# Optimization experiments

Measured on AMD Instinct MI355X. Metric: run time of the kernel, lower is better.

Reference implementation:

```python
import jax, jax.numpy as jnp
from jax import lax
import numpy as np
import math

B_SZ, SEQ, D_MODEL = 2, 2048, 2048
D_INNER, D_STATE, D_CONV, HEADS, P, CHUNK = 4096, 128, 4, 64, 64, 128
CONV_DIM = D_INNER + 2 * D_STATE
D_IN_PROJ = 2 * D_INNER + 2 * D_STATE + HEADS


def setup_inputs() -> dict:
    key = jax.random.key(0)
    ks = jax.random.split(key, 6)
    hidden_states = jax.random.normal(ks[0], (B_SZ, SEQ, D_MODEL), jnp.float32)
    W_in = jax.random.normal(ks[1], (D_IN_PROJ, D_MODEL), jnp.float32) * 0.02
    W_conv = jax.random.normal(ks[2], (CONV_DIM, 1, D_CONV), jnp.float32) * 0.2
    b_conv = jnp.zeros((CONV_DIM,), jnp.float32)
    A_log = jnp.log(jnp.arange(1, HEADS + 1, dtype=jnp.float32))
    D = jnp.ones((HEADS,), jnp.float32)
    # dt_bias init as in the torch module
    dt = jnp.exp(jax.random.uniform(ks[3], (HEADS,)) * (math.log(0.1) - math.log(0.001)) + math.log(0.001))
    dt = jnp.clip(dt, 1e-4, None)
    dt_bias = dt + jnp.log(-jnp.expm1(-dt))
    norm_weight = jnp.ones((D_INNER,), jnp.float32)
    W_out = jax.random.normal(ks[4], (D_MODEL, D_INNER), jnp.float32) * 0.02
    return {"hidden_states": hidden_states, "W_in": W_in, "W_conv": W_conv, "b_conv": b_conv,
            "A_log": A_log, "D": D, "dt_bias": dt_bias, "norm_weight": norm_weight, "W_out": W_out}


def _mamba2_core(hidden_states, W_in, W_conv, b_conv, A_log, D, dt_bias, norm_weight, W_out):
    Bsz, L, _ = hidden_states.shape
    NC = L // CHUNK
    zxbcdt = hidden_states @ W_in.T                         # [B,L,d_in_proj]
    z = zxbcdt[..., :D_INNER]
    xBC = zxbcdt[..., D_INNER:D_INNER + CONV_DIM]
    dt = zxbcdt[..., -HEADS:]
    # causal depthwise conv1d over sequence
    xc = jnp.swapaxes(xBC, 1, 2)                            # [B,C,L]
    xc = lax.conv_general_dilated(xc, W_conv, (1,), [(D_CONV - 1, 0)],
                                  feature_group_count=CONV_DIM,
                                  dimension_numbers=('NCH', 'OIH', 'NCH'))
    xc = xc + b_conv[None, :, None]
    xBC = jax.nn.silu(jnp.swapaxes(xc, 1, 2))               # [B,L,conv_dim]
    x = xBC[..., :D_INNER]
    Bm = xBC[..., D_INNER:D_INNER + D_STATE]                # num_groups=1
    Cm = xBC[..., -D_STATE:]
    dt = jax.nn.softplus(dt + dt_bias)                      # [B,L,H]; dt_limit (0,inf) is a no-op
    A = -jnp.exp(A_log)                                     # [H]
    # --- chunked SSD scan (chunk_size = CHUNK), same math as torch_ssm ---
    xch = x.reshape(Bsz, NC, CHUNK, HEADS, P)
    dtc = dt.reshape(Bsz, NC, CHUNK, HEADS)
    Bc = Bm.reshape(Bsz, NC, CHUNK, D_STATE)
    Cc = Cm.reshape(Bsz, NC, CHUNK, D_STATE)
    u = xch * dtc[..., None]                                # [b,c,l,h,p]
    dA = dtc * A                                            # [b,c,l,h]
    dA_cs = jnp.cumsum(dA, axis=2)                          # [b,c,l,h]
    # within-chunk causal attention-like term
    seg = dA_cs[:, :, :, None, :] - dA_cs[:, :, None, :, :] # [b,c,l,s,h]
    mask = jnp.tril(jnp.ones((CHUNK, CHUNK), bool))
    Lmat = jnp.exp(jnp.where(mask[None, None, :, :, None], seg, -jnp.inf))
    CB = jnp.einsum('bcln,bcsn->bcls', Cc, Bc)
    M = CB[..., None] * Lmat                                # [b,c,l,s,h]
    Y_diag = jnp.einsum('bclsh,bcshp->bclhp', M, u)
    # per-chunk final states
    decay_states = jnp.exp(dA_cs[:, :, -1:, :] - dA_cs)     # [b,c,l,h]
    states = jnp.einsum('bcln,bclh,bclhp->bchpn', Bc, decay_states, u)
    chunk_decay = jnp.exp(dA_cs[:, :, -1, :])               # [b,c,h]
    # inter-chunk recurrence over NC chunks
    def step(h, inp):
        st, cd = inp                                        # [b,h,p,n], [b,h]
        h_new = h * cd[:, :, None, None] + st
        return h_new, h                                     # emit state at chunk start
    sts = jnp.moveaxis(states, 1, 0)
    cds = jnp.moveaxis(chunk_decay, 1, 0)
    h0 = jnp.zeros((Bsz, HEADS, P, D_STATE), hidden_states.dtype)
    _, h_starts = lax.scan(step, h0, (sts, cds))
    h_starts = jnp.moveaxis(h_starts, 0, 1)                 # [b,c,h,p,n]
    state_decay_out = jnp.exp(dA_cs)                        # [b,c,l,h]
    Y_off = jnp.einsum('bcln,bclh,bchpn->bclhp', Cc, state_decay_out, h_starts)
    Y = Y_diag + Y_off + D[None, None, None, :, None] * xch
    y = Y.reshape(Bsz, L, D_INNER)
    # gated RMSNorm (gate first, then norm; group_size == d_inner)
    yg = y * jax.nn.silu(z)
    var = jnp.mean(yg * yg, axis=-1, keepdims=True)
    y = yg * lax.rsqrt(var + 1e-5) * norm_weight
    return y @ W_out.T


def reference(hidden_states, W_in, W_conv, b_conv, A_log, D, dt_bias, norm_weight, W_out):
    return _mamba2_core(hidden_states, W_in, W_conv, b_conv, A_log, D, dt_bias, norm_weight, W_out)
```

## Files before the change

kernel.cpp:

```cpp
#include <hip/hip_runtime.h>
#include <hip/hip_bf16.h>
#include <stdint.h>

typedef __bf16 bf16;
typedef __bf16 bf16x8 __attribute__((ext_vector_type(8)));
typedef __bf16 bf16x4 __attribute__((ext_vector_type(4)));
typedef float f32x4v __attribute__((ext_vector_type(4)));

#define SEQ    2048
#define DMODEL 2048
#define DI     4096
#define NH     64
#define PDIM   64
#define CHUNKL 128
#define NCH    16
#define CONVD  4352
#define DPROJ  8512
#define ZLD    8704
#define NTOK   4096
#define LP     136

__device__ __forceinline__ float sigmoid_f(float x){ return 1.f/(1.f+expf(-x)); }
__device__ __forceinline__ float silu_f(float x){ return x*sigmoid_f(x); }
__device__ __forceinline__ float softplus_f(float x){ return x > 20.f ? x : log1pf(expf(x)); }

__global__ __launch_bounds__(256) void cvt_all_kernel(const float* __restrict__ hs,
                                                      const float* __restrict__ W_in,
                                                      const float* __restrict__ W_out,
                                                      bf16* __restrict__ hsb,
                                                      bf16* __restrict__ winb,
                                                      bf16* __restrict__ woutb){
    int blk = blockIdx.x;
    if (blk < 8192){
        int i = (blk*256 + threadIdx.x)*4;
        float4 v = *(const float4*)&hs[i];
        bf16x4 o; o[0]=(bf16)v.x; o[1]=(bf16)v.y; o[2]=(bf16)v.z; o[3]=(bf16)v.w;
        *(bf16x4*)&hsb[i] = o;
    } else if (blk < 25600){
        int i = ((blk-8192)*256 + threadIdx.x)*4;
        int r = i >> 11;
        bf16x4 o;
        if (r < DPROJ){
            float4 v = *(const float4*)&W_in[i];
            o[0]=(bf16)v.x; o[1]=(bf16)v.y; o[2]=(bf16)v.z; o[3]=(bf16)v.w;
        } else {
            o[0]=(bf16)0.f; o[1]=(bf16)0.f; o[2]=(bf16)0.f; o[3]=(bf16)0.f;
        }
        *(bf16x4*)&winb[i] = o;
    } else {
        int i = ((blk-25600)*256 + threadIdx.x)*4;
        float4 v = *(const float4*)&W_out[i];
        bf16x4 o; o[0]=(bf16)v.x; o[1]=(bf16)v.y; o[2]=(bf16)v.z; o[3]=(bf16)v.w;
        *(bf16x4*)&woutb[i] = o;
    }
}

#define READ_A(BUFP, QM)                                                               \
    {                                                                                  \
        _Pragma("unroll")                                                              \
        for (int i=0;i<4;i++)                                                          \
            _Pragma("unroll")                                                          \
            for (int k2=0;k2<2;k2++)                                                   \
                af[i][k2] = *(const bf16x8*)&(BUFP)[aoff[i][k2] + (QM)*8192];          \
    }

#define READ_B(BUFP, QN, BFR)                                                          \
    {                                                                                  \
        _Pragma("unroll")                                                              \
        for (int nf=0;nf<2;nf++)                                                       \
            _Pragma("unroll")                                                          \
            for (int k2=0;k2<2;k2++)                                                   \
                BFR[nf][k2] = *(const bf16x8*)&(BUFP)[boff[nf][k2] + (QN)*8192];       \
    }

#define MMA_Q(QM, QN, BFR)                                                             \
    {                                                                                  \
        __builtin_amdgcn_s_setprio(1);                                                 \
        _Pragma("unroll")                                                              \
        for (int i=0;i<4;i++)                                                          \
            _Pragma("unroll")                                                          \
            for (int nf=0;nf<2;nf++)                                                   \
                _Pragma("unroll")                                                      \
                for (int k2=0;k2<2;k2++)                                               \
                    acc[(QM)*4+i][(QN)*2+nf] = __builtin_amdgcn_mfma_f32_16x16x32_bf16( \
                        af[i][k2], BFR[nf][k2], acc[(QM)*4+i][(QN)*2+nf], 0,0,0);      \
        __builtin_amdgcn_s_setprio(0);                                                 \
    }

#define SBAR() do { __builtin_amdgcn_sched_barrier(0);                                 \
                    __builtin_amdgcn_s_barrier();                                      \
                    asm volatile("s_waitcnt lgkmcnt(0)" ::: "memory");                 \
                    __builtin_amdgcn_sched_barrier(0); } while(0)

__global__ __launch_bounds__(512) void gemm1_kernel(const bf16* __restrict__ A,
                                                    const bf16* __restrict__ Bmat,
                                                    bf16* __restrict__ Cz,
                                                    float* __restrict__ tpart,
                                                    int NXB, int NYB, int K){
    __shared__ __align__(16) bf16 lds[2][2*16384];
    const int tid  = threadIdx.x;
    const int w    = tid >> 6;
    const int lane = tid & 63;
    const int wm   = w >> 2, wn = w & 3;

    int bid = blockIdx.x;
    int x, y, kz = 0, KT, kt0;
    if (bid < 128){
        kz = bid >> 5;
        int t32 = bid & 31;
        x = 32 + (t32 & 1);
        y = t32 >> 1;
        KT = 8; kt0 = kz*8;
    } else {
        int bid2 = bid - 128;
        int wg   = (bid2 & 7)*64 + (bid2 >> 3);
        const int SW = 8;
        int sup = wg / (SW*NYB);
        int rr  = wg % (SW*NYB);
        int x0  = sup*SW;
        int wl  = (NXB - x0 < SW) ? (NXB - x0) : SW;
        x = x0 + rr % wl;
        y = rr / wl;
        KT = K >> 6; kt0 = 0;
    }
    const int tm = y*256, tn = x*256;

    f32x4v acc[8][4];
    #pragma unroll
    for (int i=0;i<8;i++)
        #pragma unroll
        for (int j=0;j<4;j++) acc[i][j] = {0.f,0.f,0.f,0.f};
    bf16x8 af[4][2];
    bf16x8 bfr0[2][2], bfr1[2][2];

    const bf16* srcA[2][2];
    const bf16* srcB[2][2];
    #pragma unroll
    for (int r0h=0;r0h<2;r0h++)
        #pragma unroll
        for (int i=0;i<2;i++){
            int lr = r0h*128 + i*64 + (tid>>3);
            int growA = tm + ((lr>>6)&1)*128 + (lr>>7)*64 + (lr&63);
            int growB = tn + ((lr>>5)&3)*64 + (lr>>7)*32 + (lr&31);
            int gslot = (tid&7) ^ (lr&7);
            srcA[r0h][i] = A + (long)growA*K + gslot*8;
            srcB[r0h][i] = Bmat + (long)growB*K + gslot*8;
        }
    int aoff[4][2], boff[2][2];
    #pragma unroll
    for (int i=0;i<4;i++)
        #pragma unroll
        for (int k2=0;k2<2;k2++){
            int ra0 = wm*64 + i*16 + (lane&15);
            int slot = (k2*4 + (lane>>4)) ^ (ra0&7);
            aoff[i][k2] = ra0*64 + slot*8;
        }
    #pragma unroll
    for (int nf=0;nf<2;nf++)
        #pragma unroll
        for (int k2=0;k2<2;k2++){
            int rb0 = wn*32 + nf*16 + (lane&15);
            int slot = (k2*4 + (lane>>4)) ^ (rb0&7);
            boff[nf][k2] = 16384 + rb0*64 + slot*8;
        }

    auto stageA = [&](int buf, int t, int r0h){
        long koff = (long)(kt0 + t)*64;
        #pragma unroll
        for (int i=0;i<2;i++){
            bf16* dst = &lds[buf][0] + (size_t)(r0h*128 + i*64 + w*8)*64;
            __builtin_amdgcn_global_load_lds(
                (const __attribute__((address_space(1))) void*)(srcA[r0h][i] + koff),
                (__attribute__((address_space(3))) void*)dst, 16, 0, 0);
        }
    };
    auto stageB = [&](int buf, int t, int r0h){
        long koff = (long)(kt0 + t)*64;
        #pragma unroll
        for (int i=0;i<2;i++){
            bf16* dst = &lds[buf][16384] + (size_t)(r0h*128 + i*64 + w*8)*64;
            __builtin_amdgcn_global_load_lds(
                (const __attribute__((address_space(1))) void*)(srcB[r0h][i] + koff),
                (__attribute__((address_space(3))) void*)dst, 16, 0, 0);
        }
    };

    stageA(0, 0, 0); stageB(0, 0, 0); stageA(0, 0, 1); stageB(0, 0, 1);
    if (KT > 1){ stageA(1, 1, 0); stageB(1, 1, 0); stageA(1, 1, 1); stageB(1, 1, 1); }
    asm volatile("s_waitcnt vmcnt(8)" ::: "memory");
    __builtin_amdgcn_s_barrier();

    int cur = 0;
    for (int t = 0; t < KT; ++t){
        int nxt = cur ^ 1;
        const bf16* bufc = &lds[cur][0];
        READ_A(bufc, 0)
        READ_B(bufc, 0, bfr0)
        READ_B(bufc, 1, bfr1)
        if (t+1 < KT){ asm volatile("s_waitcnt vmcnt(8)" ::: "memory"); }
        else         { asm volatile("s_waitcnt vmcnt(0)" ::: "memory"); }
        SBAR();
        MMA_Q(0, 0, bfr0)
        MMA_Q(0, 1, bfr1)
        __builtin_amdgcn_sched_barrier(0);
        if (t+2 < KT){ stageA(cur, t+2, 0); stageB(cur, t+2, 0); }
        READ_A(bufc, 1)
        SBAR();
        MMA_Q(1, 0, bfr0)
        MMA_Q(1, 1, bfr1)
        __builtin_amdgcn_sched_barrier(0);
        if (t+2 < KT){ stageA(cur, t+2, 1); stageB(cur, t+2, 1); }
        cur = nxt;
    }

    const int er = (lane>>4)*4, ec = lane&15;
    #pragma unroll
    for (int mi=0;mi<8;mi++)
        #pragma unroll
        for (int ni=0;ni<4;ni++){
            long r0 = tm + wm*128 + mi*16 + er;
            int  c0 = tn + wn*64 + ni*16 + ec;
            #pragma unroll
            for (int j=0;j<4;j++){
                float val = acc[mi][ni][j];
                if (x < 32){
                    Cz[(r0+j)*ZLD + c0] = (bf16)val;
                } else {
                    tpart[((long)kz*4096 + (r0+j))*512 + (c0 - 8192)] = val;
                }
            }
        }
}

__global__ __launch_bounds__(512) void gemm256x128_kernel(const bf16* __restrict__ A,
                                                          const bf16* __restrict__ Bmat,
                                                          float* __restrict__ C,
                                                          int NXB, int NYB, int K, int ldc){
    __shared__ __align__(16) bf16 lds[3][24576];
    const int tid  = threadIdx.x;
    const int w    = tid >> 6;
    const int lane = tid & 63;
    const int wm   = w >> 2, wn = w & 3;

    int bid = blockIdx.x, nb = gridDim.x;
    int wg = (bid & 7)*(nb >> 3) + (bid >> 3);
    const int SW = 8;
    int sup = wg / (SW*NYB);
    int rr  = wg % (SW*NYB);
    int x0  = sup*SW;
    int wl  = (NXB - x0 < SW) ? (NXB - x0) : SW;
    int x   = x0 + rr % wl;
    int y   = rr / wl;
    const int tm = y*256, tn = x*128;
    const int KT = K >> 6;

    f32x4v acc[8][2];
    #pragma unroll
    for (int i=0;i<8;i++)
        #pragma unroll
        for (int j=0;j<2;j++) acc[i][j] = {0.f,0.f,0.f,0.f};
    bf16x8 af[4][2];
    bf16x8 bfr[2][2];

    const bf16* srcA[2][2];
    const bf16* srcB[2];
    #pragma unroll
    for (int r0h=0;r0h<2;r0h++)
        #pragma unroll
        for (int i=0;i<2;i++){
            int lr = r0h*128 + i*64 + (tid>>3);
            int growA = tm + ((lr>>6)&1)*128 + (lr>>7)*64 + (lr&63);
            int gslot = (tid&7) ^ (lr&7);
            srcA[r0h][i] = A + (long)growA*K + gslot*8;
        }
    #pragma unroll
    for (int i=0;i<2;i++){
        int lr = i*64 + (tid>>3);
        int growB = tn + lr;
        int gslot = (tid&7) ^ (lr&7);
        srcB[i] = Bmat + (long)growB*K + gslot*8;
    }
    int aoff[4][2], boff[2][2];
    #pragma unroll
    for (int i=0;i<4;i++)
        #pragma unroll
        for (int k2=0;k2<2;k2++){
            int ra0 = wm*64 + i*16 + (lane&15);
            int slot = (k2*4 + (lane>>4)) ^ (ra0&7);
            aoff[i][k2] = ra0*64 + slot*8;
        }
    #pragma unroll
    for (int nf=0;nf<2;nf++)
        #pragma unroll
        for (int k2=0;k2<2;k2++){
            int rb0 = wn*32 + nf*16 + (lane&15);
            int slot = (k2*4 + (lane>>4)) ^ (rb0&7);
            boff[nf][k2] = 16384 + rb0*64 + slot*8;
        }

    auto stageA = [&](int buf, int t, int r0h){
        long koff = (long)t*64;
        #pragma unroll
        for (int i=0;i<2;i++){
            bf16* dst = &lds[buf][0] + (size_t)(r0h*128 + i*64 + w*8)*64;
            __builtin_amdgcn_global_load_lds(
                (const __attribute__((address_space(1))) void*)(srcA[r0h][i] + koff),
                (__attribute__((address_space(3))) void*)dst, 16, 0, 0);
        }
    };
    auto stageB = [&](int buf, int t){
        long koff = (long)t*64;
        #pragma unroll
        for (int i=0;i<2;i++){
            bf16* dst = &lds[buf][16384] + (size_t)(i*64 + w*8)*64;
            __builtin_amdgcn_global_load_lds(
                (const __attribute__((address_space(1))) void*)(srcB[i] + koff),
                (__attribute__((address_space(3))) void*)dst, 16, 0, 0);
        }
    };

    stageA(0, 0, 0); stageA(0, 0, 1); stageB(0, 0);
    if (KT > 1){ stageA(1, 1, 0); stageA(1, 1, 1); stageB(1, 1); }
    asm volatile("s_waitcnt vmcnt(6)" ::: "memory");
    __builtin_amdgcn_s_barrier();

    int cur = 0;
    for (int t = 0; t < KT; ++t){
        int stb = cur + 2; if (stb >= 3) stb -= 3;
        const bf16* bufc = &lds[cur][0];
        READ_A(bufc, 0)
        READ_B(bufc, 0, bfr)
        if (t+2 < KT){ stageA(stb, t+2, 0); stageA(stb, t+2, 1); }
        SBAR();
        MMA_Q(0, 0, bfr)
        READ_A(bufc, 1)
        if (t+2 < KT){
            stageB(stb, t+2);
            asm volatile("s_waitcnt vmcnt(6)" ::: "memory");
        } else {
            asm volatile("s_waitcnt vmcnt(0)" ::: "memory");
        }
        SBAR();
        MMA_Q(1, 0, bfr)
        cur = (cur == 2) ? 0 : cur + 1;
    }

    const int er = (lane>>4)*4, ec = lane&15;
    #pragma unroll
    for (int mi=0;mi<8;mi++)
        #pragma unroll
        for (int ni=0;ni<2;ni++){
            long r0 = tm + wm*128 + mi*16 + er;
            int  c0 = tn + wn*32 + ni*16 + ec;
            #pragma unroll
            for (int j=0;j<4;j++)
                C[(r0+j)*ldc + c0] = acc[mi][ni][j];
        }
}

__global__ __launch_bounds__(256) void tailreduce_kernel(const float* __restrict__ p,
                                                         bf16* __restrict__ zx,
                                                         float* __restrict__ dtf){
    long i = ((long)blockIdx.x*256 + threadIdx.x)*4;
    int r = (int)(i >> 9);
    int c = (int)(i & 511);
    const long Q = (long)4096*512;
    float4 a  = *(const float4*)&p[i];
    float4 b  = *(const float4*)&p[i+Q];
    float4 cc = *(const float4*)&p[i+2*Q];
    float4 d  = *(const float4*)&p[i+3*Q];
    float s0 = a.x+b.x+cc.x+d.x, s1 = a.y+b.y+cc.y+d.y;
    float s2 = a.z+b.z+cc.z+d.z, s3 = a.w+b.w+cc.w+d.w;
    bf16x4 o; o[0]=(bf16)s0; o[1]=(bf16)s1; o[2]=(bf16)s2; o[3]=(bf16)s3;
    *(bf16x4*)&zx[(long)r*ZLD + 8192 + c] = o;
    int col = 8192 + c;
    float sv[4] = {s0,s1,s2,s3};
    #pragma unroll
    for (int j=0;j<4;j++){
        int cj = col + j;
        if (cj >= 8448 && cj < 8512) dtf[(long)r*64 + (cj-8448)] = sv[j];
    }
}

__global__ __launch_bounds__(256) void conv_silu_kernel(const bf16* __restrict__ zx,
                                                        const float* __restrict__ Wc,
                                                        const float* __restrict__ bc,
                                                        bf16* __restrict__ xc){
    int c4 = blockIdx.x*256 + threadIdx.x;
    if (c4 >= 1088) return;
    int ch = c4*4;
    int byy = blockIdx.y;
    int b = byy >> 8, t0 = (byy & 255)*8;
    float4 tap[4];
    #pragma unroll
    for (int e=0;e<4;e++) tap[e] = *(const float4*)&Wc[(ch+e)*4];
    float4 bq = *(const float4*)&bc[ch];
    float bca[4] = {bq.x, bq.y, bq.z, bq.w};
    const bf16* col = zx + (long)(b*SEQ)*ZLD + 4096 + ch;
    bf16x4 v[11];
    #pragma unroll
    for (int k=0;k<11;k++){
        int t = t0 - 3 + k;
        if (t >= 0) v[k] = *(const bf16x4*)&col[(long)t*ZLD];
        else { v[k][0]=(bf16)0.f; v[k][1]=(bf16)0.f; v[k][2]=(bf16)0.f; v[k][3]=(bf16)0.f; }
    }
    #pragma unroll
    for (int j=0;j<8;j++){
        bf16x4 o;
        #pragma unroll
        for (int e=0;e<4;e++){
            float acc = bca[e] + (float)v[j][e]*tap[e].x + (float)v[j+1][e]*tap[e].y
                               + (float)v[j+2][e]*tap[e].z + (float)v[j+3][e]*tap[e].w;
            o[e] = (bf16)silu_f(acc);
        }
        *(bf16x4*)&xc[(long)(b*SEQ + t0 + j)*CONVD + ch] = o;
    }
}

__global__ __launch_bounds__(256) void dtcum_kernel(const float* __restrict__ dtf,
                                                    const float* __restrict__ A_log,
                                                    const float* __restrict__ dt_bias,
                                                    float* __restrict__ dtv,
                                                    float* __restrict__ dacs,
                                                    float* __restrict__ cdec){
    int wid  = (blockIdx.x*256 + threadIdx.x) >> 6;
    int lane = threadIdx.x & 63;
    int h  = wid & 63, bc = wid >> 6;
    int b  = bc >> 4,  c  = bc & 15;
    float Ah   = -expf(A_log[h]);
    float bias = dt_bias[h];
    long tok0 = (long)(b*SEQ + c*CHUNKL);
    int l0 = lane*2;
    float d0 = softplus_f(dtf[(tok0+l0)*64 + h] + bias);
    float d1 = softplus_f(dtf[(tok0+l0+1)*64 + h] + bias);
    float s = (d0 + d1)*Ah;
    #pragma unroll
    for (int off=1; off<64; off<<=1){
        float t = __shfl_up(s, off, 64);
        if (lane >= off) s += t;
    }
    long base_h = (long)wid*128;
    float cs1 = s;
    float cs0 = s - d1*Ah;
    dtv[base_h+l0]   = d0;  dtv[base_h+l0+1]  = d1;
    dacs[base_h+l0]  = cs0; dacs[base_h+l0+1] = cs1;
    if (lane == 63) cdec[wid] = expf(cs1);
}

__global__ __launch_bounds__(256) void cb_mfma_kernel(const bf16* __restrict__ xc,
                                                      float* __restrict__ cb){
    __shared__ __align__(16) bf16 A1[128*LP];
    __shared__ __align__(16) bf16 B1[128*LP];
    int blk = blockIdx.x;  int b = blk>>4, c = blk&15;
    int tid = threadIdx.x;
    const int w = tid >> 6, lane = tid & 63;
    long tok0 = (long)(b*SEQ + c*CHUNKL);
    int l = tid>>1, n0 = (tid&1)*64;
    const bf16* crow = xc + tok0*CONVD + (long)l*CONVD;
    #pragma unroll
    for (int v=0;v<8;v++){
        *(bf16x8*)&A1[l*LP + n0 + v*8] = *(const bf16x8*)&crow[4224 + n0 + v*8];
        *(bf16x8*)&B1[l*LP + n0 + v*8] = *(const bf16x8*)&crow[4096 + n0 + v*8];
    }
    __syncthreads();
    f32x4v acc[2][8];
    #pragma unroll
    for (int mi=0;mi<2;mi++)
        #pragma unroll
        for (int ni=0;ni<8;ni++) acc[mi][ni] = {0.f,0.f,0.f,0.f};
    #pragma unroll
    for (int kk=0; kk<128; kk+=32){
        bf16x8 afr[2], bfr2[8];
        #pragma unroll
        for (int mi=0;mi<2;mi++)
            afr[mi] = *(const bf16x8*)&A1[(w*32 + mi*16 + (lane&15))*LP + kk + (lane>>4)*8];
        #pragma unroll
        for (int ni=0;ni<8;ni++)
            bfr2[ni] = *(const bf16x8*)&B1[(ni*16 + (lane&15))*LP + kk + (lane>>4)*8];
        #pragma unroll
        for (int mi=0;mi<2;mi++)
            #pragma unroll
            for (int ni=0;ni<8;ni++)
                acc[mi][ni] = __builtin_amdgcn_mfma_f32_16x16x32_bf16(afr[mi], bfr2[ni], acc[mi][ni], 0,0,0);
    }
    float* out = cb + (long)blk*16384;
    #pragma unroll
    for (int mi=0;mi<2;mi++)
        #pragma unroll
        for (int ni=0;ni<8;ni++){
            int r0 = w*32 + mi*16 + (lane>>4)*4;
            int c0 = ni*16 + (lane&15);
            #pragma unroll
            for (int j=0;j<4;j++) out[(long)(r0+j)*128 + c0] = acc[mi][ni][j];
        }
}

__global__ __launch_bounds__(256) void states_mfma_kernel(const bf16* __restrict__ xc,
                                                          const float* __restrict__ dtv,
                                                          const float* __restrict__ dacs,
                                                          bf16* __restrict__ states){
    __shared__ __align__(16) bf16 A1[64*LP];
    __shared__ __align__(16) bf16 B1[128*LP];
    __shared__ float wgtl[128];
    int blk = blockIdx.x;
    int h = blk & 63, bc = blk >> 6;
    int b = bc >> 4, c = bc & 15;
    int tid = threadIdx.x;
    const int w = tid >> 6, lane = tid & 63;
    long tok0 = (long)(b*SEQ + c*CHUNKL);
    long base_h = (long)blk*128;
    float cs_last = dacs[base_h + 127];
    if (tid < 128) wgtl[tid] = dtv[base_h+tid] * expf(cs_last - dacs[base_h+tid]);
    __syncthreads();
    #pragma unroll
    for (int t=0;t<4;t++){
        int l = (tid>>3) + t*32;
        int p0 = (tid&7)*8;
        bf16x8 xv = *(const bf16x8*)&xc[(tok0+l)*CONVD + h*64 + p0];
        float wv = wgtl[l];
        #pragma unroll
        for (int e=0;e<8;e++) A1[(p0+e)*LP + l] = (bf16)((float)xv[e]*wv);
    }
    {
        int l = tid>>1, n0 = (tid&1)*64;
        const bf16* brow = xc + (tok0+l)*CONVD + 4096;
        #pragma unroll
        for (int v=0;v<8;v++){
            bf16x8 bv = *(const bf16x8*)&brow[n0 + v*8];
            #pragma unroll
            for (int e=0;e<8;e++) B1[(n0+v*8+e)*LP + l] = bv[e];
        }
    }
    __syncthreads();
    f32x4v acc[8];
    #pragma unroll
    for (int ni=0;ni<8;ni++) acc[ni] = {0.f,0.f,0.f,0.f};
    #pragma unroll
    for (int kk=0; kk<128; kk+=32){
        bf16x8 afr = *(const bf16x8*)&A1[(w*16 + (lane&15))*LP + kk + (lane>>4)*8];
        #pragma unroll
        for (int ni=0;ni<8;ni++){
            bf16x8 bfr2 = *(const bf16x8*)&B1[(ni*16 + (lane&15))*LP + kk + (lane>>4)*8];
            acc[ni] = __builtin_amdgcn_mfma_f32_16x16x32_bf16(afr, bfr2, acc[ni], 0,0,0);
        }
    }
    bf16* out = states + (long)blk*8192;
    #pragma unroll
    for (int ni=0;ni<8;ni++){
        int p0 = w*16 + (lane>>4)*4;
        int n  = ni*16 + (lane&15);
        #pragma unroll
        for (int j=0;j<4;j++) out[(long)(p0+j)*128 + n] = (bf16)acc[ni][j];
    }
}

__global__ __launch_bounds__(256) void scan_kernel(const bf16* __restrict__ states,
                                                   const float* __restrict__ cdec,
                                                   bf16* __restrict__ hst){
    long gid = (long)blockIdx.x*256 + threadIdx.x;
    int n = gid & 127;
    int p = (gid >> 7) & 63;
    int h = (gid >> 13) & 63;
    int b = (int)(gid >> 19);
    float hrun = 0.f;
    for (int c=0;c<16;c++){
        long idx = ((((long)(b*16 + c)*64 + h)*64 + p)*128) + n;
        hst[idx] = (bf16)hrun;
        hrun = hrun * cdec[(b*16+c)*64 + h] + (float)states[idx];
    }
}

__global__ __launch_bounds__(256) void yfused_kernel(const bf16* __restrict__ xc,
                                                     const float* __restrict__ cb,
                                                     const bf16* __restrict__ hst,
                                                     const float* __restrict__ dtv,
                                                     const float* __restrict__ dacs,
                                                     bf16* __restrict__ Ybf){
    __shared__ __align__(16) bf16 A1[128*LP];
    __shared__ __align__(16) bf16 B1[64*LP];
    __shared__ float csl[128];
    int blk = blockIdx.x;
    int h = blk & 63, bc = blk >> 6;
    int b = bc >> 4, c = bc & 15;
    int tid = threadIdx.x;
    const int w = tid >> 6, lane = tid & 63;
    long tok0 = (long)(b*SEQ + c*CHUNKL);
    long base_h = (long)blk*128;
    if (tid < 128) csl[tid] = dacs[base_h + tid];
    __syncthreads();
    {
        int l = tid>>1, s0 = (tid&1)*64;
        float el = csl[l];
        const float* cbrow = cb + (long)bc*16384 + (long)l*128 + s0;
        #pragma unroll 8
        for (int j=0;j<64;j++){
            int s = s0 + j;
            float v = (s <= l) ? cbrow[j]*expf(el - csl[s]) : 0.f;
            A1[l*LP + s] = (bf16)v;
        }
    }
    #pragma unroll
    for (int t=0;t<4;t++){
        int s = (tid>>3) + t*32;
        int p0 = (tid&7)*8;
        bf16x8 xv = *(const bf16x8*)&xc[(tok0+s)*CONVD + h*64 + p0];
        float wv = dtv[base_h + s];
        #pragma unroll
        for (int e=0;e<8;e++) B1[(p0+e)*LP + s] = (bf16)((float)xv[e]*wv);
    }
    __syncthreads();
    f32x4v acc[2][4];
    #pragma unroll
    for (int mi=0;mi<2;mi++)
        #pragma unroll
        for (int ni=0;ni<4;ni++) acc[mi][ni] = {0.f,0.f,0.f,0.f};
    #pragma unroll
    for (int kk=0; kk<128; kk+=32){
        bf16x8 afr[2], bfr2[4];
        #pragma unroll
        for (int mi=0;mi<2;mi++)
            afr[mi] = *(const bf16x8*)&A1[(w*32 + mi*16 + (lane&15))*LP + kk + (lane>>4)*8];
        #pragma unroll
        for (int ni=0;ni<4;ni++)
            bfr2[ni] = *(const bf16x8*)&B1[(ni*16 + (lane&15))*LP + kk + (lane>>4)*8];
        #pragma unroll
        for (int mi=0;mi<2;mi++)
            #pragma unroll
            for (int ni=0;ni<4;ni++)
                acc[mi][ni] = __builtin_amdgcn_mfma_f32_16x16x32_bf16(afr[mi], bfr2[ni], acc[mi][ni], 0,0,0);
    }
    __syncthreads();
    {
        int l = tid>>1, n0 = (tid&1)*64;
        float e1 = expf(csl[l]);
        const bf16* crow = xc + (tok0+l)*CONVD + 4224;
        #pragma unroll
        for (int v=0;v<8;v++){
            bf16x8 cv = *(const bf16x8*)&crow[n0 + v*8];
            bf16x8 o;
            #pragma unroll
            for (int e=0;e<8;e++) o[e] = (bf16)((float)cv[e]*e1);
            *(bf16x8*)&A1[l*LP + n0 + v*8] = o;
        }
    }
    {
        int p = tid>>2, n0 = (tid&3)*32;
        const bf16* hrow = hst + (long)blk*8192 + (long)p*128 + n0;
        #pragma unroll
        for (int v=0;v<4;v++)
            *(bf16x8*)&B1[p*LP + n0 + v*8] = *(const bf16x8*)&hrow[v*8];
    }
    __syncthreads();
    #pragma unroll
    for (int kk=0; kk<128; kk+=32){
        bf16x8 afr[2], bfr2[4];
        #pragma unroll
        for (int mi=0;mi<2;mi++)
            afr[mi] = *(const bf16x8*)&A1[(w*32 + mi*16 + (lane&15))*LP + kk + (lane>>4)*8];
        #pragma unroll
        for (int ni=0;ni<4;ni++)
            bfr2[ni] = *(const bf16x8*)&B1[(ni*16 + (lane&15))*LP + kk + (lane>>4)*8];
        #pragma unroll
        for (int mi=0;mi<2;mi++)
            #pragma unroll
            for (int ni=0;ni<4;ni++)
                acc[mi][ni] = __builtin_amdgcn_mfma_f32_16x16x32_bf16(afr[mi], bfr2[ni], acc[mi][ni], 0,0,0);
    }
    #pragma unroll
    for (int mi=0;mi<2;mi++)
        #pragma unroll
        for (int ni=0;ni<4;ni++){
            int l0 = w*32 + mi*16 + (lane>>4)*4;
            int p  = ni*16 + (lane&15);
            #pragma unroll
            for (int j=0;j<4;j++)
                Ybf[(tok0 + l0 + j)*DI + h*64 + p] = (bf16)acc[mi][ni][j];
        }
}

__global__ __launch_bounds__(256) void gatenorm_kernel(const bf16* __restrict__ Ybf,
                                                       const bf16* __restrict__ zx,
                                                       const bf16* __restrict__ xc,
                                                       const float* __restrict__ Dp,
                                                       const float* __restrict__ nw,
                                                       bf16* __restrict__ ybn){
    __shared__ float red[4];
    int tok = blockIdx.x, tid = threadIdx.x;
    const bf16* yrow = Ybf + (long)tok*DI;
    const bf16* zrow = zx  + (long)tok*ZLD;
    const bf16* xrow = xc  + (long)tok*CONVD;
    float yg[16];
    float ss = 0.f;
    #pragma unroll
    for (int k=0;k<2;k++){
        int d = (tid + k*256)*8;
        bf16x8 yv = *(const bf16x8*)&yrow[d];
        bf16x8 zv = *(const bf16x8*)&zrow[d];
        bf16x8 xv = *(const bf16x8*)&xrow[d];
        float dh = Dp[d>>6];
        #pragma unroll
        for (int e=0;e<8;e++){
            float yy = (float)yv[e] + dh*(float)xv[e];
            float g = yy*silu_f((float)zv[e]);
            yg[k*8+e] = g;
            ss += g*g;
        }
    }
    #pragma unroll
    for (int off=32; off>0; off>>=1) ss += __shfl_down(ss, off, 64);
    if ((tid & 63) == 0) red[tid>>6] = ss;
    __syncthreads();
    float tot = red[0]+red[1]+red[2]+red[3];
    float scale = rsqrtf(tot/(float)DI + 1e-5f);
    #pragma unroll
    for (int k=0;k<2;k++){
        int d = (tid + k*256)*8;
        float4 w0 = *(const float4*)&nw[d];
        float4 w1 = *(const float4*)&nw[d+4];
        float wv[8] = {w0.x,w0.y,w0.z,w0.w,w1.x,w1.y,w1.z,w1.w};
        bf16x8 o;
        #pragma unroll
        for (int e=0;e<8;e++) o[e] = (bf16)(yg[k*8+e]*scale*wv[e]);
        *(bf16x8*)&ybn[(long)tok*DI + d] = o;
    }
}

extern "C" void kernel_launch(void* const* d_in, const int* in_sizes, int n_in,
                              void* d_out, int out_size, void* d_ws, size_t ws_size,
                              hipStream_t stream){
    const float* hs      = (const float*)d_in[0];
    const float* W_in    = (const float*)d_in[1];
    const float* W_conv  = (const float*)d_in[2];
    const float* b_conv  = (const float*)d_in[3];
    const float* A_log   = (const float*)d_in[4];
    const float* Dp      = (const float*)d_in[5];
    const float* dt_bias = (const float*)d_in[6];
    const float* nw      = (const float*)d_in[7];
    const float* W_out   = (const float*)d_in[8];
    float* out = (float*)d_out;

    char* ws = (char*)d_ws;
    const size_t OFF_ZX    = 0;
    const size_t OFF_DTF   = 71303168;
    const size_t OFF_XC    = 72351744;
    const size_t OFF_DTV   = 108003328;
    const size_t OFF_DACS  = 109051904;
    const size_t OFF_CDEC  = 110100480;
    const size_t OFF_CB    = 110108672;
    const size_t OFF_SLOTA = 112205824;
    const size_t OFF_SLOTB = 179314688;
    const size_t OFF_WOUTB = 212869120;

    bf16*  zx    = (bf16*)(ws + OFF_ZX);
    float* dtf   = (float*)(ws + OFF_DTF);
    bf16*  xc    = (bf16*)(ws + OFF_XC);
    float* dtv   = (float*)(ws + OFF_DTV);
    float* dacs  = (float*)(ws + OFF_DACS);
    float* cdec  = (float*)(ws + OFF_CDEC);
    float* cbuf  = (float*)(ws + OFF_CB);
    bf16*  hsb   = (bf16*)(ws + OFF_SLOTA);
    bf16*  winb  = (bf16*)(ws + OFF_SLOTA + 16777216);
    bf16*  states= (bf16*)(ws + OFF_SLOTA);
    bf16*  Ybf   = (bf16*)(ws + OFF_SLOTA);
    float* tpart = (float*)(ws + OFF_SLOTB);
    bf16*  hst   = (bf16*)(ws + OFF_SLOTB);
    bf16*  ybn   = (bf16*)(ws + OFF_SLOTB);
    bf16*  woutb = (bf16*)(ws + OFF_WOUTB);

    cvt_all_kernel<<<33792, 256, 0, stream>>>(hs, W_in, W_out, hsb, winb, woutb);

    gemm1_kernel<<<640, 512, 0, stream>>>(hsb, winb, zx, tpart, 32, 16, DMODEL);
    tailreduce_kernel<<<2048, 256, 0, stream>>>(tpart, zx, dtf);

    conv_silu_kernel<<<dim3(5, 512), 256, 0, stream>>>(zx, W_conv, b_conv, xc);
    dtcum_kernel<<<512, 256, 0, stream>>>(dtf, A_log, dt_bias, dtv, dacs, cdec);
    cb_mfma_kernel<<<32, 256, 0, stream>>>(xc, cbuf);
    states_mfma_kernel<<<2048, 256, 0, stream>>>(xc, dtv, dacs, states);
    scan_kernel<<<4096, 256, 0, stream>>>(states, cdec, hst);
    yfused_kernel<<<2048, 256, 0, stream>>>(xc, cbuf, hst, dtv, dacs, Ybf);
    gatenorm_kernel<<<4096, 256, 0, stream>>>(Ybf, zx, xc, Dp, nw, ybn);

    gemm256x128_kernel<<<256, 512, 0, stream>>>(ybn, woutb, out, 16, 16, DI, DMODEL);
}
```

Measured before the change: 431.3 us.

## Retile gemm1 tail blocks, merge conv and dt-cumsum kernels, share transposed B

The split-K tail of the input projection now runs as 256 separate 256x128 tiles with a simpler double-buffered loop, in place of 128 256x256 tiles that shared the main kernel's loop. The causal conv and the dt cumsum kernels are merged into one launch. cb_mfma now writes a transposed copy of B so states_mfma can load it with vector reads, and yfused skips computing the masked upper-triangle entries. The aim is better load balance and fewer launches and scattered loads, at the cost of one extra small buffer write.

Measured after the change: 373.2 us. -13.5%, faster.

```diff
diff --git a/kernel.cpp b/kernel.cpp
--- a/kernel.cpp
+++ b/kernel.cpp
@@ -102,28 +102,132 @@
     const int w    = tid >> 6;
     const int lane = tid & 63;
     const int wm   = w >> 2, wn = w & 3;
-
-    int bid = blockIdx.x;
-    int x, y, kz = 0, KT, kt0;
-    if (bid < 128){
-        kz = bid >> 5;
-        int t32 = bid & 31;
-        x = 32 + (t32 & 1);
-        y = t32 >> 1;
-        KT = 8; kt0 = kz*8;
-    } else {
-        int bid2 = bid - 128;
-        int wg   = (bid2 & 7)*64 + (bid2 >> 3);
-        const int SW = 8;
-        int sup = wg / (SW*NYB);
-        int rr  = wg % (SW*NYB);
-        int x0  = sup*SW;
-        int wl  = (NXB - x0 < SW) ? (NXB - x0) : SW;
-        x = x0 + rr % wl;
-        y = rr / wl;
-        KT = K >> 6; kt0 = 0;
-    }
+    const int bid  = blockIdx.x;
+
+    int aoff[4][2], boff[2][2];
+    #pragma unroll
+    for (int i=0;i<4;i++)
+        #pragma unroll
+        for (int k2=0;k2<2;k2++){
+            int ra0 = wm*64 + i*16 + (lane&15);
+            int slot = (k2*4 + (lane>>4)) ^ (ra0&7);
+            aoff[i][k2] = ra0*64 + slot*8;
+        }
+    #pragma unroll
+    for (int nf=0;nf<2;nf++)
+        #pragma unroll
+        for (int k2=0;k2<2;k2++){
+            int rb0 = wn*32 + nf*16 + (lane&15);
+            int slot = (k2*4 + (lane>>4)) ^ (rb0&7);
+            boff[nf][k2] = 16384 + rb0*64 + slot*8;
+        }
+    const int er = (lane>>4)*4, ec = lane&15;
+
+    if (bid < 256){
+        int kz  = bid >> 6;
+        int t64 = bid & 63;
+        const int tn2 = 8192 + (t64 & 3)*128;
+        const int tm2 = (t64 >> 2)*256;
+        const int kt0 = kz*8;
+
+        const bf16* srcA2[2][2];
+        const bf16* srcB2[2];
+        #pragma unroll
+        for (int r0h=0;r0h<2;r0h++)
+            #pragma unroll
+            for (int i=0;i<2;i++){
+                int lr = r0h*128 + i*64 + (tid>>3);
+                int growA = tm2 + ((lr>>6)&1)*128 + (lr>>7)*64 + (lr&63);
+                int gslot = (tid&7) ^ (lr&7);
+                srcA2[r0h][i] = A + (long)growA*K + gslot*8;
+            }
+        #pragma unroll
+        for (int i=0;i<2;i++){
+            int lr = i*64 + (tid>>3);
+            int gslot = (tid&7) ^ (lr&7);
+            srcB2[i] = Bmat + (long)(tn2 + lr)*K + gslot*8;
+        }
+        auto stA = [&](int buf, int t, int r0h){
+            long koff = (long)(kt0 + t)*64;
+            #pragma unroll
+            for (int i=0;i<2;i++){
+                bf16* dst = &lds[buf][0] + (size_t)(r0h*128 + i*64 + w*8)*64;
+                __builtin_amdgcn_global_load_lds(
+                    (const __attribute__((address_space(1))) void*)(srcA2[r0h][i] + koff),
+                    (__attribute__((address_space(3))) void*)dst, 16, 0, 0);
+            }
+        };
+        auto stB = [&](int buf, int t){
+            long koff = (long)(kt0 + t)*64;
+            #pragma unroll
+            for (int i=0;i<2;i++){
+                bf16* dst = &lds[buf][16384] + (size_t)(i*64 + w*8)*64;
+                __builtin_amdgcn_global_load_lds(
+                    (const __attribute__((address_space(1))) void*)(srcB2[i] + koff),
+                    (__attribute__((address_space(3))) void*)dst, 16, 0, 0);
+            }
+        };
+
+        f32x4v acc2[8][2];
+        #pragma unroll
+        for (int i=0;i<8;i++)
+            #pragma unroll
+            for (int j=0;j<2;j++) acc2[i][j] = {0.f,0.f,0.f,0.f};
+        bf16x8 af[4][2], bfr0[2][2];
+
+        stA(0,0,0); stA(0,0,1); stB(0,0);
+        __syncthreads();
+        int cur = 0;
+        for (int t=0; t<8; ++t){
+            int nxt = cur ^ 1;
+            const bf16* bufc = &lds[cur][0];
+            if (t+1 < 8){ stA(nxt,t+1,0); stA(nxt,t+1,1); stB(nxt,t+1); }
+            READ_A(bufc, 0)
+            READ_B(bufc, 0, bfr0)
+            #pragma unroll
+            for (int i=0;i<4;i++)
+                #pragma unroll
+                for (int nf=0;nf<2;nf++)
+                    #pragma unroll
+                    for (int k2=0;k2<2;k2++)
+                        acc2[i][nf] = __builtin_amdgcn_mfma_f32_16x16x32_bf16(
+                            af[i][k2], bfr0[nf][k2], acc2[i][nf], 0,0,0);
+            READ_A(bufc, 1)
+            #pragma unroll
+            for (int i=0;i<4;i++)
+                #pragma unroll
+                for (int nf=0;nf<2;nf++)
+                    #pragma unroll
+                    for (int k2=0;k2<2;k2++)
+                        acc2[4+i][nf] = __builtin_amdgcn_mfma_f32_16x16x32_bf16(
+                            af[i][k2], bfr0[nf][k2], acc2[4+i][nf], 0,0,0);
+            __syncthreads();
+            cur = nxt;
+        }
+        #pragma unroll
+        for (int mi=0;mi<8;mi++)
+            #pragma unroll
+            for (int nf=0;nf<2;nf++){
+                long r0 = tm2 + wm*128 + mi*16 + er;
+                int  c0 = tn2 + wn*32 + nf*16 + ec;
+                #pragma unroll
+                for (int j=0;j<4;j++)
+                    tpart[((long)kz*4096 + (r0+j))*512 + (c0 - 8192)] = acc2[mi][nf][j];
+            }
+        return;
+    }
+
+    int bid2 = bid - 256;
+    int wg   = (bid2 & 7)*64 + (bid2 >> 3);
+    const int SW = 8;
+    int sup = wg / (SW*NYB);
+    int rr  = wg % (SW*NYB);
+    int x0  = sup*SW;
+    int wl  = (NXB - x0 < SW) ? (NXB - x0) : SW;
+    int x   = x0 + rr % wl;
+    int y   = rr / wl;
     const int tm = y*256, tn = x*256;
+    const int KT = K >> 6;
 
     f32x4v acc[8][4];
     #pragma unroll
@@ -146,26 +250,9 @@
             srcA[r0h][i] = A + (long)growA*K + gslot*8;
             srcB[r0h][i] = Bmat + (long)growB*K + gslot*8;
         }
-    int aoff[4][2], boff[2][2];
-    #pragma unroll
-    for (int i=0;i<4;i++)
-        #pragma unroll
-        for (int k2=0;k2<2;k2++){
-            int ra0 = wm*64 + i*16 + (lane&15);
-            int slot = (k2*4 + (lane>>4)) ^ (ra0&7);
-            aoff[i][k2] = ra0*64 + slot*8;
-        }
-    #pragma unroll
-    for (int nf=0;nf<2;nf++)
-        #pragma unroll
-        for (int k2=0;k2<2;k2++){
-            int rb0 = wn*32 + nf*16 + (lane&15);
-            int slot = (k2*4 + (lane>>4)) ^ (rb0&7);
-            boff[nf][k2] = 16384 + rb0*64 + slot*8;
-        }
 
     auto stageA = [&](int buf, int t, int r0h){
-        long koff = (long)(kt0 + t)*64;
+        long koff = (long)t*64;
         #pragma unroll
         for (int i=0;i<2;i++){
             bf16* dst = &lds[buf][0] + (size_t)(r0h*128 + i*64 + w*8)*64;
@@ -175,7 +262,7 @@
         }
     };
     auto stageB = [&](int buf, int t, int r0h){
-        long koff = (long)(kt0 + t)*64;
+        long koff = (long)t*64;
         #pragma unroll
         for (int i=0;i<2;i++){
             bf16* dst = &lds[buf][16384] + (size_t)(r0h*128 + i*64 + w*8)*64;
@@ -213,7 +300,6 @@
         cur = nxt;
     }
 
-    const int er = (lane>>4)*4, ec = lane&15;
     #pragma unroll
     for (int mi=0;mi<8;mi++)
         #pragma unroll
@@ -221,14 +307,8 @@
             long r0 = tm + wm*128 + mi*16 + er;
             int  c0 = tn + wn*64 + ni*16 + ec;
             #pragma unroll
-            for (int j=0;j<4;j++){
-                float val = acc[mi][ni][j];
-                if (x < 32){
-                    Cz[(r0+j)*ZLD + c0] = (bf16)val;
-                } else {
-                    tpart[((long)kz*4096 + (r0+j))*512 + (c0 - 8192)] = val;
-                }
-            }
+            for (int j=0;j<4;j++)
+                Cz[(r0+j)*ZLD + c0] = (bf16)acc[mi][ni][j];
         }
 }
 
@@ -276,9 +356,8 @@
     #pragma unroll
     for (int i=0;i<2;i++){
         int lr = i*64 + (tid>>3);
-        int growB = tn + lr;
         int gslot = (tid&7) ^ (lr&7);
-        srcB[i] = Bmat + (long)growB*K + gslot*8;
+        srcB[i] = Bmat + (long)(tn + lr)*K + gslot*8;
     }
     int aoff[4][2], boff[2][2];
     #pragma unroll
@@ -382,73 +461,76 @@
     }
 }
 
-__global__ __launch_bounds__(256) void conv_silu_kernel(const bf16* __restrict__ zx,
-                                                        const float* __restrict__ Wc,
-                                                        const float* __restrict__ bc,
-                                                        bf16* __restrict__ xc){
-    int c4 = blockIdx.x*256 + threadIdx.x;
-    if (c4 >= 1088) return;
-    int ch = c4*4;
-    int byy = blockIdx.y;
-    int b = byy >> 8, t0 = (byy & 255)*8;
-    float4 tap[4];
-    #pragma unroll
-    for (int e=0;e<4;e++) tap[e] = *(const float4*)&Wc[(ch+e)*4];
-    float4 bq = *(const float4*)&bc[ch];
-    float bca[4] = {bq.x, bq.y, bq.z, bq.w};
-    const bf16* col = zx + (long)(b*SEQ)*ZLD + 4096 + ch;
-    bf16x4 v[11];
-    #pragma unroll
-    for (int k=0;k<11;k++){
-        int t = t0 - 3 + k;
-        if (t >= 0) v[k] = *(const bf16x4*)&col[(long)t*ZLD];
-        else { v[k][0]=(bf16)0.f; v[k][1]=(bf16)0.f; v[k][2]=(bf16)0.f; v[k][3]=(bf16)0.f; }
-    }
-    #pragma unroll
-    for (int j=0;j<8;j++){
-        bf16x4 o;
-        #pragma unroll
-        for (int e=0;e<4;e++){
-            float acc = bca[e] + (float)v[j][e]*tap[e].x + (float)v[j+1][e]*tap[e].y
-                               + (float)v[j+2][e]*tap[e].z + (float)v[j+3][e]*tap[e].w;
-            o[e] = (bf16)silu_f(acc);
-        }
-        *(bf16x4*)&xc[(long)(b*SEQ + t0 + j)*CONVD + ch] = o;
-    }
-}
-
-__global__ __launch_bounds__(256) void dtcum_kernel(const float* __restrict__ dtf,
-                                                    const float* __restrict__ A_log,
-                                                    const float* __restrict__ dt_bias,
-                                                    float* __restrict__ dtv,
-                                                    float* __restrict__ dacs,
-                                                    float* __restrict__ cdec){
-    int wid  = (blockIdx.x*256 + threadIdx.x) >> 6;
-    int lane = threadIdx.x & 63;
-    int h  = wid & 63, bc = wid >> 6;
-    int b  = bc >> 4,  c  = bc & 15;
-    float Ah   = -expf(A_log[h]);
-    float bias = dt_bias[h];
-    long tok0 = (long)(b*SEQ + c*CHUNKL);
-    int l0 = lane*2;
-    float d0 = softplus_f(dtf[(tok0+l0)*64 + h] + bias);
-    float d1 = softplus_f(dtf[(tok0+l0+1)*64 + h] + bias);
-    float s = (d0 + d1)*Ah;
-    #pragma unroll
-    for (int off=1; off<64; off<<=1){
-        float t = __shfl_up(s, off, 64);
-        if (lane >= off) s += t;
-    }
-    long base_h = (long)wid*128;
-    float cs1 = s;
-    float cs0 = s - d1*Ah;
-    dtv[base_h+l0]   = d0;  dtv[base_h+l0+1]  = d1;
-    dacs[base_h+l0]  = cs0; dacs[base_h+l0+1] = cs1;
-    if (lane == 63) cdec[wid] = expf(cs1);
+__global__ __launch_bounds__(256) void mid1_kernel(const bf16* __restrict__ zx,
+                                                   const float* __restrict__ Wc,
+                                                   const float* __restrict__ bc,
+                                                   const float* __restrict__ dtf,
+                                                   const float* __restrict__ A_log,
+                                                   const float* __restrict__ dt_bias,
+                                                   bf16* __restrict__ xc,
+                                                   float* __restrict__ dtv,
+                                                   float* __restrict__ dacs,
+                                                   float* __restrict__ cdec){
+    int blk = blockIdx.x;
+    if (blk < 2560){
+        int by = blk/5, bx = blk%5;
+        int c4 = bx*256 + threadIdx.x;
+        if (c4 >= 1088) return;
+        int ch = c4*4;
+        int b = by >> 8, t0 = (by & 255)*8;
+        float4 tap[4];
+        #pragma unroll
+        for (int e=0;e<4;e++) tap[e] = *(const float4*)&Wc[(ch+e)*4];
+        float4 bq = *(const float4*)&bc[ch];
+        float bca[4] = {bq.x, bq.y, bq.z, bq.w};
+        const bf16* col = zx + (long)(b*SEQ)*ZLD + 4096 + ch;
+        bf16x4 v[11];
+        #pragma unroll
+        for (int k=0;k<11;k++){
+            int t = t0 - 3 + k;
+            if (t >= 0) v[k] = *(const bf16x4*)&col[(long)t*ZLD];
+            else { v[k][0]=(bf16)0.f; v[k][1]=(bf16)0.f; v[k][2]=(bf16)0.f; v[k][3]=(bf16)0.f; }
+        }
+        #pragma unroll
+        for (int j=0;j<8;j++){
+            bf16x4 o;
+            #pragma unroll
+            for (int e=0;e<4;e++){
+                float acc = bca[e] + (float)v[j][e]*tap[e].x + (float)v[j+1][e]*tap[e].y
+                                   + (float)v[j+2][e]*tap[e].z + (float)v[j+3][e]*tap[e].w;
+                o[e] = (bf16)silu_f(acc);
+            }
+            *(bf16x4*)&xc[(long)(b*SEQ + t0 + j)*CONVD + ch] = o;
+        }
+    } else {
+        int wid  = ((blk-2560)*256 + threadIdx.x) >> 6;
+        int lane = threadIdx.x & 63;
+        int h  = wid & 63, bc2 = wid >> 6;
+        int b  = bc2 >> 4,  c  = bc2 & 15;
+        float Ah   = -expf(A_log[h]);
+        float bias = dt_bias[h];
+        long tok0 = (long)(b*SEQ + c*CHUNKL);
+        int l0 = lane*2;
+        float d0 = softplus_f(dtf[(tok0+l0)*64 + h] + bias);
+        float d1 = softplus_f(dtf[(tok0+l0+1)*64 + h] + bias);
+        float s = (d0 + d1)*Ah;
+        #pragma unroll
+        for (int off=1; off<64; off<<=1){
+            float t = __shfl_up(s, off, 64);
+            if (lane >= off) s += t;
+        }
+        long base_h = (long)wid*128;
+        float cs1 = s;
+        float cs0 = s - d1*Ah;
+        dtv[base_h+l0]   = d0;  dtv[base_h+l0+1]  = d1;
+        dacs[base_h+l0]  = cs0; dacs[base_h+l0+1] = cs1;
+        if (lane == 63) cdec[wid] = expf(cs1);
+    }
 }
 
 __global__ __launch_bounds__(256) void cb_mfma_kernel(const bf16* __restrict__ xc,
-                                                      float* __restrict__ cb){
+                                                      float* __restrict__ cb,
+                                                      bf16* __restrict__ BT){
     __shared__ __align__(16) bf16 A1[128*LP];
     __shared__ __align__(16) bf16 B1[128*LP];
     int blk = blockIdx.x;  int b = blk>>4, c = blk&15;
@@ -493,9 +575,21 @@
             #pragma unroll
             for (int j=0;j<4;j++) out[(long)(r0+j)*128 + c0] = acc[mi][ni][j];
         }
+    {
+        int n = tid>>1, s0 = (tid&1)*64;
+        bf16* btp = BT + (long)blk*16384 + (long)n*128 + s0;
+        #pragma unroll
+        for (int v=0;v<8;v++){
+            bf16x8 o;
+            #pragma unroll
+            for (int e=0;e<8;e++) o[e] = B1[(s0+v*8+e)*LP + n];
+            *(bf16x8*)&btp[v*8] = o;
+        }
+    }
 }
 
 __global__ __launch_bounds__(256) void states_mfma_kernel(const bf16* __restrict__ xc,
+                                                          const bf16* __restrict__ BT,
                                                           const float* __restrict__ dtv,
                                                           const float* __restrict__ dacs,
                                                           bf16* __restrict__ states){
@@ -522,14 +616,11 @@
         for (int e=0;e<8;e++) A1[(p0+e)*LP + l] = (bf16)((float)xv[e]*wv);
     }
     {
-        int l = tid>>1, n0 = (tid&1)*64;
-        const bf16* brow = xc + (tok0+l)*CONVD + 4096;
-        #pragma unroll
-        for (int v=0;v<8;v++){
-            bf16x8 bv = *(const bf16x8*)&brow[n0 + v*8];
-            #pragma unroll
-            for (int e=0;e<8;e++) B1[(n0+v*8+e)*LP + l] = bv[e];
-        }
+        int n = tid>>1, l0 = (tid&1)*64;
+        const bf16* btp = BT + (long)bc*16384 + (long)n*128 + l0;
+        #pragma unroll
+        for (int v=0;v<8;v++)
+            *(bf16x8*)&B1[n*LP + l0 + v*8] = *(const bf16x8*)&btp[v*8];
     }
     __syncthreads();
     f32x4v acc[8];
@@ -592,12 +683,11 @@
         int l = tid>>1, s0 = (tid&1)*64;
         float el = csl[l];
         const float* cbrow = cb + (long)bc*16384 + (long)l*128 + s0;
-        #pragma unroll 8
-        for (int j=0;j<64;j++){
-            int s = s0 + j;
-            float v = (s <= l) ? cbrow[j]*expf(el - csl[s]) : 0.f;
-            A1[l*LP + s] = (bf16)v;
-        }
+        int jend = l - s0; if (jend > 63) jend = 63;
+        for (int j=0; j<=jend; j++)
+            A1[l*LP + s0 + j] = (bf16)(cbrow[j]*expf(el - csl[s0+j]));
+        for (int j=jend+1; j<64; j++)
+            A1[l*LP + s0 + j] = (bf16)0.f;
     }
     #pragma unroll
     for (int t=0;t<4;t++){
@@ -763,19 +853,20 @@
     bf16*  states= (bf16*)(ws + OFF_SLOTA);
     bf16*  Ybf   = (bf16*)(ws + OFF_SLOTA);
     float* tpart = (float*)(ws + OFF_SLOTB);
+    bf16*  BTb   = (bf16*)(ws + OFF_SLOTB);
     bf16*  hst   = (bf16*)(ws + OFF_SLOTB);
     bf16*  ybn   = (bf16*)(ws + OFF_SLOTB);
     bf16*  woutb = (bf16*)(ws + OFF_WOUTB);
 
     cvt_all_kernel<<<33792, 256, 0, stream>>>(hs, W_in, W_out, hsb, winb, woutb);
 
-    gemm1_kernel<<<640, 512, 0, stream>>>(hsb, winb, zx, tpart, 32, 16, DMODEL);
+    gemm1_kernel<<<768, 512, 0, stream>>>(hsb, winb, zx, tpart, 32, 16, DMODEL);
     tailreduce_kernel<<<2048, 256, 0, stream>>>(tpart, zx, dtf);
 
-    conv_silu_kernel<<<dim3(5, 512), 256, 0, stream>>>(zx, W_conv, b_conv, xc);
-    dtcum_kernel<<<512, 256, 0, stream>>>(dtf, A_log, dt_bias, dtv, dacs, cdec);
-    cb_mfma_kernel<<<32, 256, 0, stream>>>(xc, cbuf);
-    states_mfma_kernel<<<2048, 256, 0, stream>>>(xc, dtv, dacs, states);
+    mid1_kernel<<<3072, 256, 0, stream>>>(zx, W_conv, b_conv, dtf, A_log, dt_bias,
+                                          xc, dtv, dacs, cdec);
+    cb_mfma_kernel<<<32, 256, 0, stream>>>(xc, cbuf, BTb);
+    states_mfma_kernel<<<2048, 256, 0, stream>>>(xc, BTb, dtv, dacs, states);
     scan_kernel<<<4096, 256, 0, stream>>>(states, cdec, hst);
     yfused_kernel<<<2048, 256, 0, stream>>>(xc, cbuf, hst, dtv, dacs, Ybf);
     gatenorm_kernel<<<4096, 256, 0, stream>>>(Ybf, zx, xc, Dp, nw, ybn);
```
